# Kernel optimization log

Measured on AMD Instinct MI355X. Metric: run time of the kernel, lower is better.

## Reference

```python
import jax, jax.numpy as jnp
import numpy as np

NUM_HEADS = 16
BIG_NEG = -1e9  # additive mask value for padded keys (fp32)


def setup_inputs() -> dict:
    key = jax.random.key(0)
    ks = jax.random.split(key, 12)
    T, S, B, E = 2048, 2048, 2, 1024
    bound = np.sqrt(6.0 / (E + E))  # xavier_uniform for square E x E weights
    inp = {
        'query': jax.random.normal(ks[0], (T, B, E), jnp.float32),
        'key': jax.random.normal(ks[1], (S, B, E), jnp.float32),
        'value': jax.random.normal(ks[2], (S, B, E), jnp.float32),
        'attn_mask': jax.random.normal(ks[3], (T, S), jnp.float32) * 0.1,
        'key_padding_mask': jnp.zeros((B, S), dtype=bool),
        'Wq': jax.random.uniform(ks[4], (E, E), jnp.float32, -bound, bound),
        'bq': jnp.zeros((E,), jnp.float32),
        'Wk': jax.random.uniform(ks[5], (E, E), jnp.float32, -bound, bound),
        'bk': jnp.zeros((E,), jnp.float32),
        'Wv': jax.random.uniform(ks[6], (E, E), jnp.float32, -bound, bound),
        'bv': jnp.zeros((E,), jnp.float32),
        'Wo': jax.random.uniform(ks[7], (E, E), jnp.float32, -bound, bound),
        'bo': jnp.zeros((E,), jnp.float32),
    }
    return inp


def reference(query, key, value, attn_mask, key_padding_mask,
              Wq, bq, Wk, bk, Wv, bv, Wo, bo):
    T, B, E = query.shape
    S = key.shape[0]
    H = NUM_HEADS
    d = E // H
    scale = 1.0 / jnp.sqrt(jnp.asarray(d, query.dtype))

    # projections (nn.Linear: x @ W.T + b), then split heads
    q = (query @ Wq.T + bq).reshape(T, B, H, d) * scale  # [T,B,H,d]
    k = (key @ Wk.T + bk).reshape(S, B, H, d)            # [S,B,H,d]
    v = (value @ Wv.T + bv).reshape(S, B, H, d)          # [S,B,H,d]

    # QK^T scores: [B,H,T,S]
    scores = jnp.einsum('tbhd,sbhd->bhts', q, k)

    # merge masks: additive attn_mask + key_padding_mask (True -> -inf)
    merged = attn_mask[None, None, :, :] + jnp.where(
        key_padding_mask[:, None, None, :], BIG_NEG, 0.0).astype(scores.dtype)
    scores = scores + merged

    attn = jax.nn.softmax(scores, axis=-1)  # dropout p=0 -> identity

    out = jnp.einsum('bhts,sbhd->tbhd', attn, v).reshape(T, B, E)
    return out @ Wo.T + bo  # [T,B,E]
```

## Files before the change

### kernel.cpp

```cpp
#include <hip/hip_runtime.h>
#include <hip/hip_bf16.h>

typedef unsigned short u16;
typedef __attribute__((ext_vector_type(8))) short bf16x8;
typedef __attribute__((ext_vector_type(4))) float f32x4;

#define T_DIM 2048
#define S_DIM 2048
#define B_DIM 2
#define E_DIM 1024
#define H_DIM 16
#define D_HEAD 64
#define NTOK 4096

#if __has_builtin(__builtin_amdgcn_exp2f)
#define EXP2F(x) __builtin_amdgcn_exp2f(x)
#else
#define EXP2F(x) exp2f(x)
#endif

#define GLL16(gp, lp) __builtin_amdgcn_global_load_lds((gp), (lp), 16, 0, 0)

__device__ __forceinline__ float bf2f(u16 u) {
  union { unsigned int i; float f; } v; v.i = ((unsigned int)u) << 16; return v.f;
}
__device__ __forceinline__ u16 f2bf(float f) {
  union { float f; unsigned int i; } v; v.f = f;
  unsigned int r = v.i + 0x7fffu + ((v.i >> 16) & 1u);
  return (u16)(r >> 16);
}
__device__ __forceinline__ unsigned pk2(float a, float b) {
  return (unsigned)f2bf(a) | ((unsigned)f2bf(b) << 16);
}
__device__ __forceinline__ float bfu_lo(unsigned w) {
  union { unsigned int i; float f; } v; v.i = w << 16; return v.f;
}
__device__ __forceinline__ float bfu_hi(unsigned w) {
  union { unsigned int i; float f; } v; v.i = w & 0xffff0000u; return v.f;
}
__device__ __forceinline__ uint4 loadA8(const void* A, size_t base, int bf) {
  if (bf) return *(const uint4*)&((const u16*)A)[base];
  const float* af = (const float*)A + base;
  uint4 r;
  r.x = pk2(af[0], af[1]); r.y = pk2(af[2], af[3]);
  r.z = pk2(af[4], af[5]); r.w = pk2(af[6], af[7]);
  return r;
}

__global__ void detect_dtype(const u16* q, int* flag) {
  int lane = threadIdx.x;
  float v = bf2f(q[2 * lane]);
  bool ok = (v < 16.f) && (v > -16.f);
  unsigned long long b = __ballot(ok);
  if (lane == 0) *flag = (b == ~0ull) ? 1 : 0;
}

#define PARAM_BLOCKS 16400
__launch_bounds__(256)
__global__ void prep_a(const void* Wq, const void* Wk, const void* Wv, const void* Wo,
                       const void* bq, const void* bk, const void* bv, const void* bo,
                       u16* wqkv, u16* wo, float* b3, float* bof,
                       const void* Q, const void* Kk, const void* V,
                       u16* qb, u16* kb, u16* vb,
                       const int* flag) {
  const int bf = *flag;
  const int bid = blockIdx.x;
  if (bid < PARAM_BLOCKS) {
    const int W = E_DIM * E_DIM;
    int idx = bid * 256 + threadIdx.x;
    if (idx < 4 * W) {
      int which = idx / W, i = idx - which * W;
      const void* src = which == 0 ? Wq : which == 1 ? Wk : which == 2 ? Wv : Wo;
      float v = bf ? bf2f(((const u16*)src)[i]) : ((const float*)src)[i];
      if (which == 0) v *= 0.125f;
      if (which < 3) wqkv[idx] = f2bf(v);
      else           wo[i] = f2bf(v);
    } else {
      int j = idx - 4 * W;
      if (j < 4 * E_DIM) {
        int which = j / E_DIM, i = j - which * E_DIM;
        const void* src = which == 0 ? bq : which == 1 ? bk : which == 2 ? bv : bo;
        float v = bf ? bf2f(((const u16*)src)[i]) : ((const float*)src)[i];
        if (which == 0) v *= 0.125f;
        if (which < 3) b3[j] = v;
        else           bof[i] = v;
      }
    }
  } else {
    const size_t W = (size_t)NTOK * E_DIM;
    size_t e8 = ((size_t)(bid - PARAM_BLOCKS) * 256 + threadIdx.x) * 8;
    int which = (int)(e8 / W);
    size_t i = e8 - (size_t)which * W;
    const void* src = which == 0 ? Q : which == 1 ? Kk : V;
    u16* dst = which == 0 ? qb : which == 1 ? kb : vb;
    *(uint4*)&dst[i] = loadA8(src, i, bf);
  }
}

__launch_bounds__(256)
__global__ void prep_b(const u16* __restrict__ vp, u16* __restrict__ vt,
                       const void* __restrict__ mask, const unsigned char* __restrict__ kpm,
                       u16* __restrict__ Mc, const int* __restrict__ flag) {
  const int bid = blockIdx.x;
  if (bid < 1024) {
    __shared__ unsigned int t[64 * 65];
    const int tid = threadIdx.x;
    const int s0 = (bid & 31) * 64;
    const int bh = bid >> 5;
    const int b = bh / H_DIM, h = bh % H_DIM;
    {
      int sr = tid >> 2, cq = (tid & 3) * 16;
      const u16* src = &vp[((size_t)(s0 + sr) * B_DIM + b) * E_DIM + h * 64 + cq];
#pragma unroll
      for (int j = 0; j < 16; j++) t[(cq + j) * 65 + sr] = src[j];
    }
    __syncthreads();
    {
      int d = tid >> 2, sq = (tid & 3) * 16;
      u16* dst = &vt[((size_t)bh * 64 + d) * S_DIM + s0 + sq];
      uint4 o0, o1;
      o0.x = (t[d*65+sq+0] & 0xffffu) | (t[d*65+sq+1] << 16);
      o0.y = (t[d*65+sq+2] & 0xffffu) | (t[d*65+sq+3] << 16);
      o0.z = (t[d*65+sq+4] & 0xffffu) | (t[d*65+sq+5] << 16);
      o0.w = (t[d*65+sq+6] & 0xffffu) | (t[d*65+sq+7] << 16);
      o1.x = (t[d*65+sq+8] & 0xffffu) | (t[d*65+sq+9] << 16);
      o1.y = (t[d*65+sq+10] & 0xffffu) | (t[d*65+sq+11] << 16);
      o1.z = (t[d*65+sq+12] & 0xffffu) | (t[d*65+sq+13] << 16);
      o1.w = (t[d*65+sq+14] & 0xffffu) | (t[d*65+sq+15] << 16);
      *(uint4*)&dst[0] = o0;
      *(uint4*)&dst[8] = o1;
    }
  } else {
    const float L2E = 1.44269504f;
    const int bf = *flag;
    size_t e8 = ((size_t)(bid - 1024) * 256 + threadIdx.x) * 8;
    int b = (int)(e8 / ((size_t)T_DIM * S_DIM));
    size_t rem = e8 - (size_t)b * T_DIM * S_DIM;
    int tt = (int)(rem / S_DIM), s = (int)(rem - (size_t)tt * S_DIM);
    const unsigned char* kb = &kpm[(size_t)b * S_DIM + s];
    uint4 o;
    if (bf) {
      const u16* m8 = &((const u16*)mask)[(size_t)tt * S_DIM + s];
      o.x = pk2((bf2f(m8[0]) + (kb[0] ? -1e9f : 0.f)) * L2E,
                (bf2f(m8[1]) + (kb[1] ? -1e9f : 0.f)) * L2E);
      o.y = pk2((bf2f(m8[2]) + (kb[2] ? -1e9f : 0.f)) * L2E,
                (bf2f(m8[3]) + (kb[3] ? -1e9f : 0.f)) * L2E);
      o.z = pk2((bf2f(m8[4]) + (kb[4] ? -1e9f : 0.f)) * L2E,
                (bf2f(m8[5]) + (kb[5] ? -1e9f : 0.f)) * L2E);
      o.w = pk2((bf2f(m8[6]) + (kb[6] ? -1e9f : 0.f)) * L2E,
                (bf2f(m8[7]) + (kb[7] ? -1e9f : 0.f)) * L2E);
    } else {
      const float* mf = (const float*)mask + (size_t)tt * S_DIM + s;
      o.x = pk2((mf[0] + (kb[0] ? -1e9f : 0.f)) * L2E,
                (mf[1] + (kb[1] ? -1e9f : 0.f)) * L2E);
      o.y = pk2((mf[2] + (kb[2] ? -1e9f : 0.f)) * L2E,
                (mf[3] + (kb[3] ? -1e9f : 0.f)) * L2E);
      o.z = pk2((mf[4] + (kb[4] ? -1e9f : 0.f)) * L2E,
                (mf[5] + (kb[5] ? -1e9f : 0.f)) * L2E);
      o.w = pk2((mf[6] + (kb[6] ? -1e9f : 0.f)) * L2E,
                (mf[7] + (kb[7] ? -1e9f : 0.f)) * L2E);
    }
    *(uint4*)&Mc[e8] = o;
  }
}

__launch_bounds__(256, 3)
__global__ void gemm_qkv(const u16* __restrict__ Qb2, const u16* __restrict__ Kb2,
                         const u16* __restrict__ Vb2, const u16* __restrict__ W3,
                         const float* __restrict__ b3,
                         u16* __restrict__ qp, u16* __restrict__ kp, u16* __restrict__ vp) {
  __shared__ alignas(16) u16 As[128 * 64];
  __shared__ alignas(16) u16 Bs[128 * 64];
  const int tid = threadIdx.x;
  const int wave = tid >> 6, lane = tid & 63;
  const int g = lane >> 4, c = lane & 15;
  const int wy = wave >> 1, wx = wave & 1;
  const int which = blockIdx.x >> 3;
  const u16* A = which == 0 ? Qb2 : which == 1 ? Kb2 : Vb2;
  u16* dst = which == 0 ? qp : which == 1 ? kp : vp;
  const int m0 = blockIdx.y * 128, n0 = blockIdx.x * 128;
  const int K = E_DIM;

  const int swr = lane >> 3;
  const int swb = (lane & 7) ^ swr;
  const u16* Ag = &A [(size_t)(m0 + wave * 8 + swr) * K + swb * 8];
  const u16* Bg = &W3[(size_t)(n0 + wave * 8 + swr) * K + swb * 8];

  f32x4 acc[4][4] = {};
  for (int kc = 0; kc < K; kc += 64) {
#pragma unroll
    for (int i = 0; i < 4; i++) {
      GLL16(&Ag[(size_t)(i * 32) * K + kc], &As[(wave * 8 + i * 32) * 64]);
      GLL16(&Bg[(size_t)(i * 32) * K + kc], &Bs[(wave * 8 + i * 32) * 64]);
    }
    __syncthreads();
#pragma unroll
    for (int ks = 0; ks < 2; ks++) {
      const int kb = (((ks << 2) | g) ^ (c & 7)) * 8;
      bf16x8 av0 = *(const bf16x8*)&As[(wy * 64 +  0 + c) * 64 + kb];
      bf16x8 av1 = *(const bf16x8*)&As[(wy * 64 + 16 + c) * 64 + kb];
      bf16x8 av2 = *(const bf16x8*)&As[(wy * 64 + 32 + c) * 64 + kb];
      bf16x8 av3 = *(const bf16x8*)&As[(wy * 64 + 48 + c) * 64 + kb];
      bf16x8 bv0 = *(const bf16x8*)&Bs[(wx * 64 +  0 + c) * 64 + kb];
      bf16x8 bv1 = *(const bf16x8*)&Bs[(wx * 64 + 16 + c) * 64 + kb];
      bf16x8 bv2 = *(const bf16x8*)&Bs[(wx * 64 + 32 + c) * 64 + kb];
      bf16x8 bv3 = *(const bf16x8*)&Bs[(wx * 64 + 48 + c) * 64 + kb];
      acc[0][0] = __builtin_amdgcn_mfma_f32_16x16x32_bf16(av0, bv0, acc[0][0], 0, 0, 0);
      acc[0][1] = __builtin_amdgcn_mfma_f32_16x16x32_bf16(av0, bv1, acc[0][1], 0, 0, 0);
      acc[0][2] = __builtin_amdgcn_mfma_f32_16x16x32_bf16(av0, bv2, acc[0][2], 0, 0, 0);
      acc[0][3] = __builtin_amdgcn_mfma_f32_16x16x32_bf16(av0, bv3, acc[0][3], 0, 0, 0);
      acc[1][0] = __builtin_amdgcn_mfma_f32_16x16x32_bf16(av1, bv0, acc[1][0], 0, 0, 0);
      acc[1][1] = __builtin_amdgcn_mfma_f32_16x16x32_bf16(av1, bv1, acc[1][1], 0, 0, 0);
      acc[1][2] = __builtin_amdgcn_mfma_f32_16x16x32_bf16(av1, bv2, acc[1][2], 0, 0, 0);
      acc[1][3] = __builtin_amdgcn_mfma_f32_16x16x32_bf16(av1, bv3, acc[1][3], 0, 0, 0);
      acc[2][0] = __builtin_amdgcn_mfma_f32_16x16x32_bf16(av2, bv0, acc[2][0], 0, 0, 0);
      acc[2][1] = __builtin_amdgcn_mfma_f32_16x16x32_bf16(av2, bv1, acc[2][1], 0, 0, 0);
      acc[2][2] = __builtin_amdgcn_mfma_f32_16x16x32_bf16(av2, bv2, acc[2][2], 0, 0, 0);
      acc[2][3] = __builtin_amdgcn_mfma_f32_16x16x32_bf16(av2, bv3, acc[2][3], 0, 0, 0);
      acc[3][0] = __builtin_amdgcn_mfma_f32_16x16x32_bf16(av3, bv0, acc[3][0], 0, 0, 0);
      acc[3][1] = __builtin_amdgcn_mfma_f32_16x16x32_bf16(av3, bv1, acc[3][1], 0, 0, 0);
      acc[3][2] = __builtin_amdgcn_mfma_f32_16x16x32_bf16(av3, bv2, acc[3][2], 0, 0, 0);
      acc[3][3] = __builtin_amdgcn_mfma_f32_16x16x32_bf16(av3, bv3, acc[3][3], 0, 0, 0);
    }
    __syncthreads();
  }
#pragma unroll
  for (int mi = 0; mi < 4; mi++)
#pragma unroll
    for (int ni = 0; ni < 4; ni++)
#pragma unroll
      for (int r = 0; r < 4; r++) {
        int row = m0 + wy * 64 + mi * 16 + g * 4 + r;
        int col = n0 + wx * 64 + ni * 16 + c;
        int inner = col & (E_DIM - 1);
        dst[(size_t)row * E_DIM + inner] = f2bf(acc[mi][ni][r] + b3[col]);
      }
}

__launch_bounds__(256, 2)
__global__ void gemm_o(const u16* __restrict__ Aa, const u16* __restrict__ Bw,
                       const float* __restrict__ bias, void* __restrict__ C,
                       int out_f32) {
  __shared__ alignas(16) u16 As[64 * 64];
  __shared__ alignas(16) u16 Bs[128 * 64];
  const int tid = threadIdx.x;
  const int wave = tid >> 6, lane = tid & 63;
  const int g = lane >> 4, c = lane & 15;
  const int wy = wave >> 1, wx = wave & 1;
  const int m0 = blockIdx.y * 64, n0 = blockIdx.x * 128;
  const int K = E_DIM, N = E_DIM;

  const int swr = lane >> 3;
  const int swb = (lane & 7) ^ swr;
  const u16* Ag = &Aa[(size_t)(m0 + wave * 8 + swr) * K + swb * 8];
  const u16* Bg = &Bw[(size_t)(n0 + wave * 8 + swr) * K + swb * 8];

  f32x4 acc[2][4] = {};
  for (int kc = 0; kc < K; kc += 64) {
#pragma unroll
    for (int i = 0; i < 2; i++)
      GLL16(&Ag[(size_t)(i * 32) * K + kc], &As[(wave * 8 + i * 32) * 64]);
#pragma unroll
    for (int i = 0; i < 4; i++)
      GLL16(&Bg[(size_t)(i * 32) * K + kc], &Bs[(wave * 8 + i * 32) * 64]);
    __syncthreads();
#pragma unroll
    for (int ks = 0; ks < 2; ks++) {
      const int kb = (((ks << 2) | g) ^ (c & 7)) * 8;
      bf16x8 av0 = *(const bf16x8*)&As[(wy * 32 +  0 + c) * 64 + kb];
      bf16x8 av1 = *(const bf16x8*)&As[(wy * 32 + 16 + c) * 64 + kb];
      bf16x8 bv0 = *(const bf16x8*)&Bs[(wx * 64 +  0 + c) * 64 + kb];
      bf16x8 bv1 = *(const bf16x8*)&Bs[(wx * 64 + 16 + c) * 64 + kb];
      bf16x8 bv2 = *(const bf16x8*)&Bs[(wx * 64 + 32 + c) * 64 + kb];
      bf16x8 bv3 = *(const bf16x8*)&Bs[(wx * 64 + 48 + c) * 64 + kb];
      acc[0][0] = __builtin_amdgcn_mfma_f32_16x16x32_bf16(av0, bv0, acc[0][0], 0, 0, 0);
      acc[0][1] = __builtin_amdgcn_mfma_f32_16x16x32_bf16(av0, bv1, acc[0][1], 0, 0, 0);
      acc[0][2] = __builtin_amdgcn_mfma_f32_16x16x32_bf16(av0, bv2, acc[0][2], 0, 0, 0);
      acc[0][3] = __builtin_amdgcn_mfma_f32_16x16x32_bf16(av0, bv3, acc[0][3], 0, 0, 0);
      acc[1][0] = __builtin_amdgcn_mfma_f32_16x16x32_bf16(av1, bv0, acc[1][0], 0, 0, 0);
      acc[1][1] = __builtin_amdgcn_mfma_f32_16x16x32_bf16(av1, bv1, acc[1][1], 0, 0, 0);
      acc[1][2] = __builtin_amdgcn_mfma_f32_16x16x32_bf16(av1, bv2, acc[1][2], 0, 0, 0);
      acc[1][3] = __builtin_amdgcn_mfma_f32_16x16x32_bf16(av1, bv3, acc[1][3], 0, 0, 0);
    }
    __syncthreads();
  }
#pragma unroll
  for (int mi = 0; mi < 2; mi++)
#pragma unroll
    for (int ni = 0; ni < 4; ni++)
#pragma unroll
      for (int r = 0; r < 4; r++) {
        int row = m0 + wy * 32 + mi * 16 + g * 4 + r;
        int col = n0 + wx * 64 + ni * 16 + c;
        float v = acc[mi][ni][r] + bias[col];
        size_t idx = (size_t)row * N + col;
        if (out_f32) ((float*)C)[idx] = v;
        else         ((u16*)C)[idx] = f2bf(v);
      }
}

__launch_bounds__(256, 4)
__global__ void flash_attn(const u16* __restrict__ Qb, const u16* __restrict__ Kb,
                           const u16* __restrict__ Vtg, const u16* __restrict__ Mc,
                           u16* __restrict__ ctx) {
  __shared__ alignas(16) u16 Ks[64 * 72];
  __shared__ alignas(16) u16 Vs[64 * 72];
  __shared__ alignas(16) u16 MP[64 * 72];
  const int tid = threadIdx.x;
  const int wave = tid >> 6, lane = tid & 63;
  const int g = lane >> 4, c = lane & 15;
  const int bh = blockIdx.x;
  const int t0 = blockIdx.y * 64;
  const int b = bh / H_DIM, h = bh % H_DIM;
  const size_t hoff = (size_t)h * D_HEAD;
  const float L2E = 1.44269504f;
  const u16* mc = &Mc[((size_t)b * T_DIM + t0) * S_DIM];
  const int rr = tid >> 3, oo = (tid & 7) * 8;

  *(uint4*)&Ks[(rr)      * 72 + oo] =
      *(const uint4*)&Qb[((size_t)(t0 + rr)      * B_DIM + b) * E_DIM + hoff + oo];
  *(uint4*)&Ks[(rr + 32) * 72 + oo] =
      *(const uint4*)&Qb[((size_t)(t0 + rr + 32) * B_DIM + b) * E_DIM + hoff + oo];
  __syncthreads();
  const int arow = wave * 16 + c;
  bf16x8 q0 = *(const bf16x8*)&Ks[arow * 72 + g * 8];
  bf16x8 q1 = *(const bf16x8*)&Ks[arow * 72 + 32 + g * 8];

  uint4 pk0, pk1, pv0, pv1, pm0, pm1;
  pk0 = *(const uint4*)&Kb[((size_t)(rr)      * B_DIM + b) * E_DIM + hoff + oo];
  pk1 = *(const uint4*)&Kb[((size_t)(rr + 32) * B_DIM + b) * E_DIM + hoff + oo];
  pv0 = *(const uint4*)&Vtg[((size_t)bh * 64 + rr)      * S_DIM + oo];
  pv1 = *(const uint4*)&Vtg[((size_t)bh * 64 + rr + 32) * S_DIM + oo];
  pm0 = *(const uint4*)&mc[(size_t)(rr)      * S_DIM + oo];
  pm1 = *(const uint4*)&mc[(size_t)(rr + 32) * S_DIM + oo];
  __syncthreads();

  f32x4 O[4] = {};
  float rsum = 0.f;
  const int trow = arow * 72;

  for (int s0 = 0; s0 < S_DIM; s0 += 64) {
    *(uint4*)&Ks[(rr)      * 72 + oo] = pk0;
    *(uint4*)&Ks[(rr + 32) * 72 + oo] = pk1;
    *(uint4*)&Vs[(rr)      * 72 + oo] = pv0;
    *(uint4*)&Vs[(rr + 32) * 72 + oo] = pv1;
    *(uint4*)&MP[(rr)      * 72 + oo] = pm0;
    *(uint4*)&MP[(rr + 32) * 72 + oo] = pm1;
    __syncthreads();
    if (s0 + 64 < S_DIM) {
      int s2 = s0 + 64;
      pk0 = *(const uint4*)&Kb[((size_t)(s2 + rr)      * B_DIM + b) * E_DIM + hoff + oo];
      pk1 = *(const uint4*)&Kb[((size_t)(s2 + rr + 32) * B_DIM + b) * E_DIM + hoff + oo];
      pv0 = *(const uint4*)&Vtg[((size_t)bh * 64 + rr)      * S_DIM + s2 + oo];
      pv1 = *(const uint4*)&Vtg[((size_t)bh * 64 + rr + 32) * S_DIM + s2 + oo];
      pm0 = *(const uint4*)&mc[(size_t)(rr)      * S_DIM + s2 + oo];
      pm1 = *(const uint4*)&mc[(size_t)(rr + 32) * S_DIM + s2 + oo];
    }

    f32x4 sc[4] = {};
    __builtin_amdgcn_s_setprio(1);
#pragma unroll
    for (int n = 0; n < 4; n++) {
      bf16x8 k0 = *(const bf16x8*)&Ks[(n * 16 + c) * 72 + g * 8];
      bf16x8 k1 = *(const bf16x8*)&Ks[(n * 16 + c) * 72 + 32 + g * 8];
      sc[n] = __builtin_amdgcn_mfma_f32_16x16x32_bf16(k0, q0, sc[n], 0, 0, 0);
      sc[n] = __builtin_amdgcn_mfma_f32_16x16x32_bf16(k1, q1, sc[n], 0, 0, 0);
    }
    __builtin_amdgcn_s_setprio(0);
#pragma unroll
    for (int n = 0; n < 4; n++) {
      uint2 mw = *(const uint2*)&MP[trow + n * 16 + g * 4];
      float p0 = EXP2F(fmaf(sc[n][0], L2E, bfu_lo(mw.x)));
      float p1 = EXP2F(fmaf(sc[n][1], L2E, bfu_hi(mw.x)));
      float p2 = EXP2F(fmaf(sc[n][2], L2E, bfu_lo(mw.y)));
      float p3 = EXP2F(fmaf(sc[n][3], L2E, bfu_hi(mw.y)));
      rsum += (p0 + p1) + (p2 + p3);
      *(unsigned*)&MP[trow + n * 16 + g * 4]     = pk2(p0, p1);
      *(unsigned*)&MP[trow + n * 16 + g * 4 + 2] = pk2(p2, p3);
    }
    bf16x8 p0 = *(const bf16x8*)&MP[arow * 72 + g * 8];
    bf16x8 p1 = *(const bf16x8*)&MP[arow * 72 + 32 + g * 8];
    __builtin_amdgcn_s_setprio(1);
#pragma unroll
    for (int n = 0; n < 4; n++) {
      bf16x8 v0 = *(const bf16x8*)&Vs[(n * 16 + c) * 72 + g * 8];
      bf16x8 v1 = *(const bf16x8*)&Vs[(n * 16 + c) * 72 + 32 + g * 8];
      O[n] = __builtin_amdgcn_mfma_f32_16x16x32_bf16(p0, v0, O[n], 0, 0, 0);
      O[n] = __builtin_amdgcn_mfma_f32_16x16x32_bf16(p1, v1, O[n], 0, 0, 0);
    }
    __builtin_amdgcn_s_setprio(0);
    __syncthreads();
  }
  float l = rsum;
  l += __shfl_xor(l, 16, 64);
  l += __shfl_xor(l, 32, 64);
  float rl = 1.f / l;
#pragma unroll
  for (int r = 0; r < 4; r++) {
    float rlr = __shfl(rl, g * 4 + r, 64);
    int t = t0 + wave * 16 + g * 4 + r;
#pragma unroll
    for (int n = 0; n < 4; n++) {
      int dcol = n * 16 + c;
      ctx[((size_t)t * B_DIM + b) * E_DIM + hoff + dcol] = f2bf(O[n][r] * rlr);
    }
  }
}

extern "C" void kernel_launch(void* const* d_in, const int* in_sizes, int n_in,
                              void* d_out, int out_size, void* d_ws, size_t ws_size,
                              hipStream_t stream) {
  const void* query = d_in[0];
  const void* key   = d_in[1];
  const void* value = d_in[2];
  const void* amask = d_in[3];
  const unsigned char* kpm = (const unsigned char*)d_in[4];
  const void* Wq = d_in[5];  const void* bq = d_in[6];
  const void* Wk = d_in[7];  const void* bk = d_in[8];
  const void* Wv = d_in[9];  const void* bv = d_in[10];
  const void* Wo = d_in[11]; const void* bo = d_in[12];

  int out_f32 = 0;
  {
    hipDeviceptr_t base = nullptr; size_t sz = 0;
    if (hipMemGetAddressRange(&base, &sz, (hipDeviceptr_t)d_out) == hipSuccess && sz) {
      size_t avail = sz - (size_t)((char*)d_out - (char*)base);
      size_t need_f32 = (size_t)out_size * 4;
      if (avail >= need_f32 && avail <= need_f32 + need_f32 / 2) out_f32 = 1;
    }
  }

  char* ws = (char*)d_ws;
  size_t off = 0;
  auto alloc = [&](size_t bytes) {
    void* p = ws + off;
    off += (bytes + 255) & ~(size_t)255;
    return p;
  };
  int*   flag = (int*)  alloc(256);
  u16*   qp   = (u16*)  alloc((size_t)NTOK * E_DIM * 2);
  u16*   kp   = (u16*)  alloc((size_t)NTOK * E_DIM * 2);
  u16*   vp   = (u16*)  alloc((size_t)NTOK * E_DIM * 2);
  u16*   vt   = (u16*)  alloc((size_t)NTOK * E_DIM * 2);
  u16*   Mcb  = (u16*)  alloc((size_t)B_DIM * T_DIM * S_DIM * 2);
  u16*   wqkv = (u16*)  alloc((size_t)3 * E_DIM * E_DIM * 2);
  u16*   wo   = (u16*)  alloc((size_t)E_DIM * E_DIM * 2);
  float* b3   = (float*)alloc(3 * E_DIM * 4);
  float* bof  = (float*)alloc(E_DIM * 4);
  if (off > ws_size) return;

  u16* qb  = vt;
  u16* kb2 = Mcb;
  u16* vb2 = Mcb + (size_t)NTOK * E_DIM;

  detect_dtype<<<1, 64, 0, stream>>>((const u16*)query, flag);

  prep_a<<<PARAM_BLOCKS + 6144, 256, 0, stream>>>(
      Wq, Wk, Wv, Wo, bq, bk, bv, bo, wqkv, wo, b3, bof,
      query, key, value, qb, kb2, vb2, flag);

  gemm_qkv<<<dim3(3 * E_DIM / 128, NTOK / 128), 256, 0, stream>>>(
      qb, kb2, vb2, wqkv, b3, qp, kp, vp);

  prep_b<<<1024 + 4096, 256, 0, stream>>>(vp, vt, amask, kpm, Mcb, flag);

  u16* ctx = vp;
  flash_attn<<<dim3(B_DIM * H_DIM, T_DIM / 64), 256, 0, stream>>>(qp, kp, vt, Mcb, ctx);

  gemm_o<<<dim3(E_DIM / 128, NTOK / 64), 256, 0, stream>>>(ctx, wo, bof, d_out, out_f32);
}
```

Baseline: 276.7 us.

## Enlarge flash attention query tile to 128 rows with 8 waves per block

Each flash-attention block now covers 128 query rows using 512 threads instead of 64 rows with 256 threads. Every K/V tile staged in shared memory is reused by twice as many waves, which halves global K/V traffic per query row and the number of blocks. The cost is a larger shared mask/probability buffer, fewer blocks in the grid (512), and a higher register and LDS footprint under launch_bounds(512,4), which may lower occupancy. The epilogue (not shown) must index with the new 128-row tile; it is assumed to still match.

```diff
diff --git a/kernel.cpp b/kernel.cpp
--- a/kernel.cpp
+++ b/kernel.cpp
@@ -299,40 +299,39 @@
       }
 }
 
-__launch_bounds__(256, 4)
+__launch_bounds__(512, 4)
 __global__ void flash_attn(const u16* __restrict__ Qb, const u16* __restrict__ Kb,
                            const u16* __restrict__ Vtg, const u16* __restrict__ Mc,
                            u16* __restrict__ ctx) {
   __shared__ alignas(16) u16 Ks[64 * 72];
   __shared__ alignas(16) u16 Vs[64 * 72];
-  __shared__ alignas(16) u16 MP[64 * 72];
+  __shared__ alignas(16) u16 MP[128 * 72];
   const int tid = threadIdx.x;
   const int wave = tid >> 6, lane = tid & 63;
   const int g = lane >> 4, c = lane & 15;
   const int bh = blockIdx.x;
-  const int t0 = blockIdx.y * 64;
+  const int t0 = blockIdx.y * 128;
   const int b = bh / H_DIM, h = bh % H_DIM;
   const size_t hoff = (size_t)h * D_HEAD;
   const float L2E = 1.44269504f;
   const u16* mc = &Mc[((size_t)b * T_DIM + t0) * S_DIM];
   const int rr = tid >> 3, oo = (tid & 7) * 8;
-
-  *(uint4*)&Ks[(rr)      * 72 + oo] =
+  const int mr = tid >> 2, mo = (tid & 3) * 16;
+
+  *(uint4*)&MP[(rr)      * 72 + oo] =
       *(const uint4*)&Qb[((size_t)(t0 + rr)      * B_DIM + b) * E_DIM + hoff + oo];
-  *(uint4*)&Ks[(rr + 32) * 72 + oo] =
-      *(const uint4*)&Qb[((size_t)(t0 + rr + 32) * B_DIM + b) * E_DIM + hoff + oo];
+  *(uint4*)&MP[(rr + 64) * 72 + oo] =
+      *(const uint4*)&Qb[((size_t)(t0 + rr + 64) * B_DIM + b) * E_DIM + hoff + oo];
   __syncthreads();
   const int arow = wave * 16 + c;
-  bf16x8 q0 = *(const bf16x8*)&Ks[arow * 72 + g * 8];
-  bf16x8 q1 = *(const bf16x8*)&Ks[arow * 72 + 32 + g * 8];
-
-  uint4 pk0, pk1, pv0, pv1, pm0, pm1;
-  pk0 = *(const uint4*)&Kb[((size_t)(rr)      * B_DIM + b) * E_DIM + hoff + oo];
-  pk1 = *(const uint4*)&Kb[((size_t)(rr + 32) * B_DIM + b) * E_DIM + hoff + oo];
-  pv0 = *(const uint4*)&Vtg[((size_t)bh * 64 + rr)      * S_DIM + oo];
-  pv1 = *(const uint4*)&Vtg[((size_t)bh * 64 + rr + 32) * S_DIM + oo];
-  pm0 = *(const uint4*)&mc[(size_t)(rr)      * S_DIM + oo];
-  pm1 = *(const uint4*)&mc[(size_t)(rr + 32) * S_DIM + oo];
+  bf16x8 q0 = *(const bf16x8*)&MP[arow * 72 + g * 8];
+  bf16x8 q1 = *(const bf16x8*)&MP[arow * 72 + 32 + g * 8];
+
+  uint4 pk0, pv0, pm0, pm1;
+  pk0 = *(const uint4*)&Kb[((size_t)(rr) * B_DIM + b) * E_DIM + hoff + oo];
+  pv0 = *(const uint4*)&Vtg[((size_t)bh * 64 + rr) * S_DIM + oo];
+  pm0 = *(const uint4*)&mc[(size_t)mr * S_DIM + mo];
+  pm1 = *(const uint4*)&mc[(size_t)mr * S_DIM + mo + 8];
   __syncthreads();
 
   f32x4 O[4] = {};
@@ -340,21 +339,17 @@
   const int trow = arow * 72;
 
   for (int s0 = 0; s0 < S_DIM; s0 += 64) {
-    *(uint4*)&Ks[(rr)      * 72 + oo] = pk0;
-    *(uint4*)&Ks[(rr + 32) * 72 + oo] = pk1;
-    *(uint4*)&Vs[(rr)      * 72 + oo] = pv0;
-    *(uint4*)&Vs[(rr + 32) * 72 + oo] = pv1;
-    *(uint4*)&MP[(rr)      * 72 + oo] = pm0;
-    *(uint4*)&MP[(rr + 32) * 72 + oo] = pm1;
+    *(uint4*)&Ks[rr * 72 + oo] = pk0;
+    *(uint4*)&Vs[rr * 72 + oo] = pv0;
+    *(uint4*)&MP[mr * 72 + mo]     = pm0;
+    *(uint4*)&MP[mr * 72 + mo + 8] = pm1;
     __syncthreads();
     if (s0 + 64 < S_DIM) {
       int s2 = s0 + 64;
-      pk0 = *(const uint4*)&Kb[((size_t)(s2 + rr)      * B_DIM + b) * E_DIM + hoff + oo];
-      pk1 = *(const uint4*)&Kb[((size_t)(s2 + rr + 32) * B_DIM + b) * E_DIM + hoff + oo];
-      pv0 = *(const uint4*)&Vtg[((size_t)bh * 64 + rr)      * S_DIM + s2 + oo];
-      pv1 = *(const uint4*)&Vtg[((size_t)bh * 64 + rr + 32) * S_DIM + s2 + oo];
-      pm0 = *(const uint4*)&mc[(size_t)(rr)      * S_DIM + s2 + oo];
-      pm1 = *(const uint4*)&mc[(size_t)(rr + 32) * S_DIM + s2 + oo];
+      pk0 = *(const uint4*)&Kb[((size_t)(s2 + rr) * B_DIM + b) * E_DIM + hoff + oo];
+      pv0 = *(const uint4*)&Vtg[((size_t)bh * 64 + rr) * S_DIM + s2 + oo];
+      pm0 = *(const uint4*)&mc[(size_t)mr * S_DIM + s2 + mo];
+      pm1 = *(const uint4*)&mc[(size_t)mr * S_DIM + s2 + mo + 8];
     }
 
     f32x4 sc[4] = {};
@@ -378,8 +373,8 @@
       *(unsigned*)&MP[trow + n * 16 + g * 4]     = pk2(p0, p1);
       *(unsigned*)&MP[trow + n * 16 + g * 4 + 2] = pk2(p2, p3);
     }
-    bf16x8 p0 = *(const bf16x8*)&MP[arow * 72 + g * 8];
-    bf16x8 p1 = *(const bf16x8*)&MP[arow * 72 + 32 + g * 8];
+    bf16x8 p0 = *(const bf16x8*)&MP[trow + g * 8];
+    bf16x8 p1 = *(const bf16x8*)&MP[trow + 32 + g * 8];
     __builtin_amdgcn_s_setprio(1);
 #pragma unroll
     for (int n = 0; n < 4; n++) {
@@ -465,7 +460,7 @@
   prep_b<<<1024 + 4096, 256, 0, stream>>>(vp, vt, amask, kpm, Mcb, flag);
 
   u16* ctx = vp;
-  flash_attn<<<dim3(B_DIM * H_DIM, T_DIM / 64), 256, 0, stream>>>(qp, kp, vt, Mcb, ctx);
+  flash_attn<<<dim3(B_DIM * H_DIM, T_DIM / 128), 512, 0, stream>>>(qp, kp, vt, Mcb, ctx);
 
   gemm_o<<<dim3(E_DIM / 128, NTOK / 64), 256, 0, stream>>>(ctx, wo, bof, d_out, out_f32);
 }
```

Result: faster. 269.2 us (-2.7%).
